# Kernel tuning notes

Hardware: AMD Instinct MI355X
Metric: run time of the kernel (lower is better)

## Reference

```python
import jax, jax.numpy as jnp
import numpy as np

B, S, D, H = 4, 1024, 1024, 16
DK = D // H


def setup_inputs() -> dict:
    key = jax.random.key(0)
    ks = jax.random.split(key, 13)
    s = 1.0 / np.sqrt(D)
    return {
        "query": jax.random.normal(ks[0], (B, S, D), jnp.float32),
        "key": jax.random.normal(ks[1], (B, S, D), jnp.float32),
        "value": jax.random.normal(ks[2], (B, S, D), jnp.float32),
        "mask": jax.random.randint(ks[3], (B, H, S, S), 0, 2).astype(bool),
        "Wq": jax.random.normal(ks[4], (D, D), jnp.float32) * s,
        "bq": jnp.zeros((D,), jnp.float32),
        "Wk": jax.random.normal(ks[5], (D, D), jnp.float32) * s,
        "bk": jnp.zeros((D,), jnp.float32),
        "Wv": jax.random.normal(ks[6], (D, D), jnp.float32) * s,
        "bv": jnp.zeros((D,), jnp.float32),
        "Wo": jax.random.normal(ks[7], (D, D), jnp.float32) * s,
        "bo": jnp.zeros((D,), jnp.float32),
    }


def reference(query, key, value, mask, Wq, bq, Wk, bk, Wv, bv, Wo, bo):
    b = query.shape[0]
    # QKV projections, split heads: [B,S,D] -> [B,H,S,DK]
    q = (query @ Wq + bq).reshape(b, -1, H, DK).transpose(0, 2, 1, 3)
    k = (key @ Wk + bk).reshape(b, -1, H, DK).transpose(0, 2, 1, 3)
    v = (value @ Wv + bv).reshape(b, -1, H, DK).transpose(0, 2, 1, 3)
    # scaled dot-product attention with explicit [B,H,Sq,Sk] scores
    scores = jnp.einsum("bhqd,bhkd->bhqk", q, k) / jnp.sqrt(jnp.float32(DK))
    scores = jnp.where(mask, -jnp.inf, scores)
    attn_weights = jax.nn.softmax(scores, axis=-1)
    attn_out = jnp.einsum("bhqk,bhkd->bhqd", attn_weights, v)
    # merge heads and project out; dropout is identity in eval mode
    attn_out = attn_out.transpose(0, 2, 1, 3).reshape(b, -1, D)
    out = attn_out @ Wo + bo
    return out, attn_weights
```

## Files before the change

### kernel.cpp

```cpp
#include <hip/hip_runtime.h>

typedef __attribute__((ext_vector_type(8))) __bf16   bf16x8;
typedef __attribute__((ext_vector_type(4))) __bf16   bf16x4;
typedef __attribute__((ext_vector_type(8))) _Float16 halfx8;
typedef __attribute__((ext_vector_type(4))) float    floatx4;
typedef __attribute__((ext_vector_type(4))) int      intx4;

#define S_  1024
#define D_  1024
#define H_  16
#define DK_ 64
#define B_  4
#define M_  4096

__device__ __forceinline__ void gload_lds16(const void* g, void* l) {
  __builtin_amdgcn_global_load_lds(
      (const __attribute__((address_space(1))) unsigned int*)g,
      (__attribute__((address_space(3))) unsigned int*)l, 16, 0, 0);
}

__global__ __launch_bounds__(256) void prep(
    const float* __restrict__ q, const float* __restrict__ k,
    const float* __restrict__ v, __bf16* __restrict__ X,
    const float* __restrict__ W0, const float* __restrict__ W1,
    const float* __restrict__ W2, const float* __restrict__ W3,
    __bf16* __restrict__ WT, const unsigned char* __restrict__ m,
    int* __restrict__ flag)
{
  __shared__ __align__(16) unsigned char shb[9216];
  const int bid = blockIdx.x;
  const int t = threadIdx.x;
  if (bid < 6144) {
    const int z = bid >> 11;
    const int bx = bid & 2047;
    const float* src = (z == 0) ? q : (z == 1) ? k : v;
    __bf16* dst = X + (size_t)z * 4194304;
    const size_t idx = ((size_t)bx * 256 + t) * 8;
    floatx4 a = *(const floatx4*)(src + idx);
    floatx4 b = *(const floatx4*)(src + idx + 4);
    bf16x8 o;
#pragma unroll
    for (int j = 0; j < 4; ++j) { o[j] = (__bf16)a[j]; o[4 + j] = (__bf16)b[j]; }
    *(bf16x8*)(dst + idx) = o;
  } else if (bid < 7168) {
    const int g = bid - 6144;
    const int z = g >> 8, yy = (g >> 4) & 15, xx = g & 15;
    const float* W = (z == 0) ? W0 : (z == 1) ? W1 : (z == 2) ? W2 : W3;
    __bf16* O = WT + (size_t)z * (D_ * (size_t)D_);
    __bf16* T = (__bf16*)shb;
    const int r0 = yy * 64, c0 = xx * 64;
#pragma unroll
    for (int it = 0; it < 4; ++it) {
      int idx = t * 4 + it * 1024;
      int r = idx >> 6, c = idx & 63;
      floatx4 a = *(const floatx4*)(W + (size_t)(r0 + r) * D_ + c0 + c);
      bf16x4 o;
#pragma unroll
      for (int j = 0; j < 4; ++j) o[j] = (__bf16)a[j];
      *(bf16x4*)(&T[r * 72 + c]) = o;
    }
    __syncthreads();
#pragma unroll
    for (int it = 0; it < 2; ++it) {
      int idx = t * 8 + it * 2048;
      int orow = idx >> 6, oc = idx & 63;
      bf16x8 vv;
#pragma unroll
      for (int j = 0; j < 8; ++j) vv[j] = T[(oc + j) * 72 + orow];
      *(bf16x8*)(O + (size_t)(c0 + orow) * D_ + (r0 + oc)) = vv;
    }
  } else {
    unsigned* sacc = (unsigned*)shb;
    unsigned acc = 0;
    for (int i = t; i < 4096; i += 256)
      if (i & 3) acc |= m[i];
    sacc[t] = acc;
    __syncthreads();
    if (t == 0) {
      unsigned tot = 0;
      for (int i = 0; i < 256; ++i) tot |= sacc[i];
      flag[0] = tot ? 1 : 0;
    }
  }
}

template <int MODE>
__device__ __forceinline__ void gemm_body(
    const __bf16* __restrict__ X, const __bf16* __restrict__ WT,
    const float* __restrict__ bias, void* __restrict__ outp, __bf16* sh,
    const int m0, const int n0)
{
  __bf16* As = sh;
  __bf16* Bs = sh + 128 * 64;
  const int t = threadIdx.x;
  const int w = t >> 6, lane = t & 63, quad = lane >> 4, cl = lane & 15;
  const int wm = w >> 1, wn = w & 1;
  const int srow = lane >> 3, scol = (lane & 7) * 8;

  floatx4 acc[4][4];
#pragma unroll
  for (int i = 0; i < 4; ++i)
#pragma unroll
    for (int j = 0; j < 4; ++j) acc[i][j] = (floatx4){0.f, 0.f, 0.f, 0.f};

  for (int kt = 0; kt < 16; ++kt) {
    const int k0 = kt * 64;
    __syncthreads();
#pragma unroll
    for (int it = 0; it < 4; ++it) {
      const int ch = it * 4 + w;
      gload_lds16(X  + (size_t)(m0 + ch * 8 + srow) * D_ + k0 + scol, As + ch * 512);
      gload_lds16(WT + (size_t)(n0 + ch * 8 + srow) * D_ + k0 + scol, Bs + ch * 512);
    }
    __syncthreads();
#pragma unroll
    for (int ks = 0; ks < 2; ++ks) {
      bf16x8 a[4], b[4];
#pragma unroll
      for (int mt = 0; mt < 4; ++mt)
        a[mt] = *(const bf16x8*)(&As[(wm * 64 + mt * 16 + cl) * 64 + ks * 32 + quad * 8]);
#pragma unroll
      for (int nt = 0; nt < 4; ++nt)
        b[nt] = *(const bf16x8*)(&Bs[(wn * 64 + nt * 16 + cl) * 64 + ks * 32 + quad * 8]);
#pragma unroll
      for (int mt = 0; mt < 4; ++mt)
#pragma unroll
        for (int nt = 0; nt < 4; ++nt)
          acc[mt][nt] = __builtin_amdgcn_mfma_f32_16x16x32_bf16(a[mt], b[nt], acc[mt][nt], 0, 0, 0);
    }
  }

  if (MODE <= 2) {
#pragma unroll
    for (int mt = 0; mt < 4; ++mt)
#pragma unroll
      for (int nt = 0; nt < 4; ++nt) {
        const int nl = n0 + wn * 64 + nt * 16 + cl;
        const float bv = bias[nl];
#pragma unroll
        for (int r = 0; r < 4; ++r) {
          const int ml = m0 + wm * 64 + mt * 16 + quad * 4 + r;
          float v = acc[mt][nt][r] + bv;
          if (MODE == 0) {
            ((float*)outp)[(size_t)ml * D_ + nl] = v;
          } else {
            if (MODE == 1) v *= 0.125f;
            const int bb = ml >> 10, ss = ml & 1023, hh = nl >> 6, dd = nl & 63;
            ((_Float16*)outp)[(size_t)((bb * H_ + hh) * S_ + ss) * DK_ + dd] = (_Float16)v;
          }
        }
      }
  } else {
    __syncthreads();
    __bf16* T = sh + w * (64 * 72);
    const int hbase = n0 + wn * 64;
#pragma unroll
    for (int mt = 0; mt < 4; ++mt)
#pragma unroll
      for (int nt = 0; nt < 4; ++nt) {
        const int nl = hbase + nt * 16 + cl;
        const float bv = bias[nl];
        const int dk = nt * 16 + cl;
#pragma unroll
        for (int r = 0; r < 4; ++r) {
          const int sl = mt * 16 + quad * 4 + r;
          T[dk * 72 + sl] = (__bf16)(acc[mt][nt][r] + bv);
        }
      }
    __syncthreads();
    const int bb = m0 >> 10;
    const int hh = hbase >> 6;
    __bf16* out = (__bf16*)outp;
#pragma unroll
    for (int i = 0; i < 8; ++i) {
      int idx = lane * 8 + i * 512;
      int dk = idx >> 6, sl = idx & 63;
      bf16x8 v = *(const bf16x8*)(&T[dk * 72 + sl]);
      int sg = (m0 & 1023) + wm * 64 + sl;
      *(bf16x8*)(out + (size_t)((bb * H_ + hh) * DK_ + dk) * S_ + sg) = v;
    }
  }
}

__global__ __launch_bounds__(256) void gemm_qkv(
    const __bf16* __restrict__ Xbf, const __bf16* __restrict__ wt,
    const float* __restrict__ bq, const float* __restrict__ bk,
    const float* __restrict__ bv,
    void* __restrict__ Qo, void* __restrict__ Ko, void* __restrict__ Vto)
{
  __shared__ __bf16 sh[18432];
  const int z = blockIdx.z;
  const int m0 = blockIdx.x * 128, n0 = blockIdx.y * 128;
  if (z == 0)      gemm_body<1>(Xbf,               wt,               bq, Qo,  sh, m0, n0);
  else if (z == 1) gemm_body<2>(Xbf + 4194304,     wt + 1048576,     bk, Ko,  sh, m0, n0);
  else             gemm_body<3>(Xbf + 2 * 4194304, wt + 2 * 1048576, bv, Vto, sh, m0, n0);
}

__global__ __launch_bounds__(256) void epilogue(
    const __bf16* __restrict__ AO, const __bf16* __restrict__ WT,
    const float* __restrict__ bo, float* __restrict__ outO,
    float* __restrict__ attnW, const __bf16* __restrict__ pp,
    const float* __restrict__ l)
{
  __shared__ __bf16 sh[18432];
  const int bid = blockIdx.x;
  if (bid < 256) {
    gemm_body<0>(AO, WT, bo, (void*)outO, sh, (bid & 31) * 128, (bid >> 5) * 128);
  } else {
    const int t = threadIdx.x;
    const int g = bid - 256;
    const int row = g * 2 + (t >> 7);
    const int c = (t & 127) * 8;
    const float lv = l[row];
    const float rl = (lv > 0.f) ? 1.0f / lv : 0.f;
    bf16x8 v = *(const bf16x8*)(pp + (size_t)row * S_ + c);
    floatx4 lo, hi;
#pragma unroll
    for (int j = 0; j < 4; ++j) { lo[j] = (float)v[j] * rl; hi[j] = (float)v[4 + j] * rl; }
    *(floatx4*)(attnW + (size_t)row * S_ + c) = lo;
    *(floatx4*)(attnW + (size_t)row * S_ + c + 4) = hi;
  }
}

__global__ __launch_bounds__(256, 4) void attn_kernel(
    const _Float16* __restrict__ Q, const _Float16* __restrict__ K,
    const __bf16* __restrict__ Vt, const unsigned char* __restrict__ maskB,
    const int* __restrict__ mflag, float* __restrict__ attnW,
    __bf16* __restrict__ pp, __bf16* __restrict__ AO,
    float* __restrict__ lout, const int sflag)
{
  __shared__ __align__(16) unsigned char smem[36864];
  _Float16*      Qs  = (_Float16*)smem;
  unsigned char* Ms  = smem;
  _Float16*      Ks  = (_Float16*)(smem + 9216);
  __bf16*        Vts = (__bf16*)(smem + 18432);
  __bf16*        Ps  = (__bf16*)(smem + 27648);

  const int t = threadIdx.x;
  const int w = t >> 6, lane = t & 63, quad = lane >> 4, cl = lane & 15;
  const int o = blockIdx.x + blockIdx.y * 16;
  const int f = (o & 7) * 128 + (o >> 3);
  const int q0 = (f & 15) * 64;
  const int bh = f >> 4;
  const bool mbyte = (*mflag != 0);
  const int* maskI = (const int*)maskB;
  const long maskbase = (long)bh * S_ * S_;

  {
    const _Float16* g = Q + (size_t)(bh * S_ + q0) * DK_;
#pragma unroll
    for (int it = 0; it < 2; ++it) {
      int idx = t * 8 + it * 2048;
      *(halfx8*)(&Qs[(idx >> 6) * 72 + (idx & 63)]) = *(const halfx8*)(g + idx);
    }
  }

  halfx8 kreg0, kreg1;
  bf16x8 vreg0, vreg1;
  intx4  mregs[4];
  const _Float16* Kbase  = K  + (size_t)bh * S_ * DK_;
  const __bf16*   Vbase  = Vt + (size_t)bh * DK_ * S_;

#define LOAD_TILE(KT)                                                              \
  {                                                                                \
    const int k0_ = (KT) * 64;                                                     \
    const _Float16* gk = Kbase + (size_t)k0_ * DK_;                                \
    kreg0 = *(const halfx8*)(gk + t * 8);                                          \
    kreg1 = *(const halfx8*)(gk + t * 8 + 2048);                                   \
    const __bf16* gv = Vbase + k0_;                                                \
    vreg0 = *(const bf16x8*)(gv + (size_t)(t >> 3) * S_ + (t & 7) * 8);            \
    vreg1 = *(const bf16x8*)(gv + (size_t)((t >> 3) + 32) * S_ + (t & 7) * 8);     \
    if (mbyte) {                                                                   \
      mregs[0] = *(const intx4*)(maskB + maskbase +                                \
                   (size_t)(q0 + (t >> 2)) * S_ + k0_ + (t & 3) * 16);             \
    } else {                                                                       \
      const int* mrowp = maskI + maskbase + (size_t)(q0 + (t >> 2)) * S_ + k0_ +   \
                         (t & 3) * 16;                                             \
      _Pragma("unroll")                                                            \
      for (int it_ = 0; it_ < 4; ++it_)                                            \
        mregs[it_] = *(const intx4*)(mrowp + it_ * 4);                             \
    }                                                                              \
  }

  LOAD_TILE(0);
  __syncthreads();
  const halfx8 a0 = *(const halfx8*)(&Qs[(w * 16 + cl) * 72 + quad * 8]);
  const halfx8 a1 = *(const halfx8*)(&Qs[(w * 16 + cl) * 72 + 32 + quad * 8]);

  float lacc[4] = {0.f, 0.f, 0.f, 0.f};
  floatx4 acc_o[4];
#pragma unroll
  for (int i = 0; i < 4; ++i) acc_o[i] = (floatx4){0.f, 0.f, 0.f, 0.f};
  __bf16* Psw = Ps + w * (16 * 72);

  for (int kt = 0; kt < 16; ++kt) {
    const int k0 = kt * 64;
    __syncthreads();

    *(halfx8*)(&Ks[(t >> 3) * 72 + (t & 7) * 8])        = kreg0;
    *(halfx8*)(&Ks[((t >> 3) + 32) * 72 + (t & 7) * 8]) = kreg1;
    *(bf16x8*)(&Vts[(t >> 3) * 72 + (t & 7) * 8])        = vreg0;
    *(bf16x8*)(&Vts[((t >> 3) + 32) * 72 + (t & 7) * 8]) = vreg1;
    {
      unsigned m16 = 0;
      if (mbyte) {
#pragma unroll
        for (int i = 0; i < 4; ++i) {
          unsigned v = (unsigned)mregs[0][i];
          m16 |= ((v & 0x000000ffu) ? 1u : 0u) << (i * 4 + 0);
          m16 |= ((v & 0x0000ff00u) ? 1u : 0u) << (i * 4 + 1);
          m16 |= ((v & 0x00ff0000u) ? 1u : 0u) << (i * 4 + 2);
          m16 |= ((v & 0xff000000u) ? 1u : 0u) << (i * 4 + 3);
        }
      } else {
#pragma unroll
        for (int it = 0; it < 4; ++it)
#pragma unroll
          for (int j = 0; j < 4; ++j)
            m16 |= (mregs[it][j] ? 1u : 0u) << (it * 4 + j);
      }
      ((unsigned short*)Ms)[(t >> 2) * 4 + (t & 3)] = (unsigned short)m16;
    }
    __syncthreads();

    unsigned long long mrow[4];
#pragma unroll
    for (int r = 0; r < 4; ++r)
      mrow[r] = ((const unsigned long long*)Ms)[w * 16 + quad * 4 + r];

    if (kt < 15) LOAD_TILE(kt + 1);

#pragma unroll
    for (int nt = 0; nt < 4; ++nt) {
      floatx4 s = (floatx4){0.f, 0.f, 0.f, 0.f};
      halfx8 b0 = *(const halfx8*)(&Ks[(nt * 16 + cl) * 72 + quad * 8]);
      halfx8 b1 = *(const halfx8*)(&Ks[(nt * 16 + cl) * 72 + 32 + quad * 8]);
      __builtin_amdgcn_s_setprio(1);
      s = __builtin_amdgcn_mfma_f32_16x16x32_f16(a0, b0, s, 0, 0, 0);
      s = __builtin_amdgcn_mfma_f32_16x16x32_f16(a1, b1, s, 0, 0, 0);
      __builtin_amdgcn_s_setprio(0);
#pragma unroll
      for (int r = 0; r < 4; ++r) {
        const int mk = (int)((mrow[r] >> (nt * 16 + cl)) & 1ull);
        float sv = s[r];
        sv = (sv < 25.f) ? sv : 25.f;
        float p = mk ? 0.0f : __expf(sv);
        __bf16 pb = (__bf16)p;
        lacc[r] += (float)pb;
        Psw[(quad * 4 + r) * 72 + nt * 16 + cl] = pb;
      }
    }

    __builtin_amdgcn_s_setprio(1);
#pragma unroll
    for (int ks = 0; ks < 2; ++ks) {
      bf16x8 a = *(const bf16x8*)(&Psw[cl * 72 + ks * 32 + quad * 8]);
#pragma unroll
      for (int nt2 = 0; nt2 < 4; ++nt2) {
        bf16x8 b = *(const bf16x8*)(&Vts[(nt2 * 16 + cl) * 72 + ks * 32 + quad * 8]);
        acc_o[nt2] = __builtin_amdgcn_mfma_f32_16x16x32_bf16(a, b, acc_o[nt2], 0, 0, 0);
      }
    }
    __builtin_amdgcn_s_setprio(0);

    if (sflag) {
      __bf16* g = pp + ((size_t)(bh * S_ + q0 + w * 16)) * S_ + k0;
#pragma unroll
      for (int i = 0; i < 2; ++i) {
        int idx = lane * 8 + i * 512;
        int r = idx >> 6, c = idx & 63;
        *(bf16x8*)(g + (size_t)r * S_ + c) = *(const bf16x8*)(&Psw[r * 72 + c]);
      }
    } else {
      float* g = attnW + ((long)(bh * S_ + q0 + w * 16)) * S_ + k0;
#pragma unroll
      for (int i = 0; i < 2; ++i) {
        int idx = lane * 8 + i * 512;
        int r = idx >> 6, c = idx & 63;
        bf16x8 v = *(const bf16x8*)(&Psw[r * 72 + c]);
        floatx4 lo, hi;
#pragma unroll
        for (int j = 0; j < 4; ++j) { lo[j] = (float)v[j]; hi[j] = (float)v[4 + j]; }
        *(floatx4*)(g + (long)r * S_ + c) = lo;
        *(floatx4*)(g + (long)r * S_ + c + 4) = hi;
      }
    }
  }
#undef LOAD_TILE

  const int bb = bh >> 4, hh = bh & 15;
#pragma unroll
  for (int r = 0; r < 4; ++r) {
    float v = lacc[r];
    v += __shfl_xor(v, 1); v += __shfl_xor(v, 2);
    v += __shfl_xor(v, 4); v += __shfl_xor(v, 8);
    const int rowg = q0 + w * 16 + quad * 4 + r;
    if (cl == 0) lout[bh * S_ + rowg] = v;
    const float rl = (v > 0.f) ? 1.0f / v : 0.f;
#pragma unroll
    for (int nt2 = 0; nt2 < 4; ++nt2) {
      float o2 = acc_o[nt2][r] * rl;
      AO[(size_t)(bb * S_ + rowg) * D_ + hh * DK_ + nt2 * 16 + cl] = (__bf16)o2;
    }
  }
}

__global__ __launch_bounds__(256) void norm_inplace(float* __restrict__ attnW,
                                                    const float* __restrict__ l)
{
  const int row = blockIdx.x;
  const float lv = l[row];
  const float rl = (lv > 0.f) ? 1.0f / lv : 0.f;
  const size_t base = (size_t)row * S_ + threadIdx.x * 4;
  floatx4 v = *(const floatx4*)(attnW + base);
#pragma unroll
  for (int j = 0; j < 4; ++j) v[j] *= rl;
  *(floatx4*)(attnW + base) = v;
}

__global__ __launch_bounds__(256) void gemm_out(
    const __bf16* __restrict__ X, const __bf16* __restrict__ WT,
    const float* __restrict__ bias, float* __restrict__ outp)
{
  __shared__ __bf16 sh[18432];
  gemm_body<0>(X, WT, bias, (void*)outp, sh, blockIdx.x * 128, blockIdx.y * 128);
}

extern "C" void kernel_launch(void* const* d_in, const int* in_sizes, int n_in,
                              void* d_out, int out_size, void* d_ws, size_t ws_size,
                              hipStream_t stream)
{
  (void)in_sizes; (void)n_in; (void)out_size;
  const float* query = (const float*)d_in[0];
  const float* key   = (const float*)d_in[1];
  const float* value = (const float*)d_in[2];
  const unsigned char* mask = (const unsigned char*)d_in[3];
  const float* Wq = (const float*)d_in[4];
  const float* bq = (const float*)d_in[5];
  const float* Wk = (const float*)d_in[6];
  const float* bk = (const float*)d_in[7];
  const float* Wv = (const float*)d_in[8];
  const float* bv = (const float*)d_in[9];
  const float* Wo = (const float*)d_in[10];
  const float* bo = (const float*)d_in[11];

  __bf16* ws = (__bf16*)d_ws;
  __bf16*   wt   = ws;
  _Float16* Qws  = (_Float16*)(ws + 4  * 1048576);
  _Float16* Kws  = (_Float16*)(ws + 8  * 1048576);
  __bf16*   Vtws = ws + 12 * 1048576;
  __bf16*   AOws = ws + 16 * 1048576;
  __bf16*   Xbf  = ws + 20 * 1048576;
  float*    lws  = (float*)(ws + 32 * 1048576);
  int*      mfl  = (int*)(ws + 32 * 1048576 + 131072);
  __bf16*   pp   = ws + 33 * 1048576;

  const int sflag = (ws_size >= 97ULL * 1048576ULL * 2ULL) ? 1 : 0;

  float* outO  = (float*)d_out;
  float* attnW = outO + 4 * 1048576;

  prep<<<7169, 256, 0, stream>>>(query, key, value, Xbf, Wq, Wk, Wv, Wo, wt, mask, mfl);
  gemm_qkv<<<dim3(32, 8, 3), 256, 0, stream>>>(Xbf, wt, bq, bk, bv,
                                               (void*)Qws, (void*)Kws, (void*)Vtws);
  attn_kernel<<<dim3(16, 64), 256, 0, stream>>>(Qws, Kws, Vtws, mask, mfl,
                                                attnW, pp, AOws, lws, sflag);
  if (sflag) {
    epilogue<<<33024, 256, 0, stream>>>(AOws, wt + 3 * 1048576, bo, outO, attnW, pp, lws);
  } else {
    norm_inplace<<<65536, 256, 0, stream>>>(attnW, lws);
    gemm_out<<<dim3(32, 8), 256, 0, stream>>>(AOws, wt + 3 * 1048576, bo, outO);
  }
}
```

Baseline: 679.1 us.

## Keep full unnormalized P row tile in LDS and write normalized attention weights directly

The attention kernel now keeps the whole 64x1024 bf16 probability tile in LDS (about 148KB) instead of a small per-step buffer. After the key loop it normalizes each row by its reciprocal sum and writes final fp32 attention weights once. This removes the bf16 scratch round trip (or the fp32 write plus in-place renormalization pass) and the separate epilogue/norm kernel. In exchange, the LDS footprint limits each CU to one block with four waves, which cuts occupancy and latency hiding in the attention loop, and the output-projection GEMM now runs as a separate launch.

```diff
diff --git a/kernel.cpp b/kernel.cpp
--- a/kernel.cpp
+++ b/kernel.cpp
@@ -196,45 +196,27 @@
   else             gemm_body<3>(Xbf + 2 * 4194304, wt + 2 * 1048576, bv, Vto, sh, m0, n0);
 }
 
-__global__ __launch_bounds__(256) void epilogue(
-    const __bf16* __restrict__ AO, const __bf16* __restrict__ WT,
-    const float* __restrict__ bo, float* __restrict__ outO,
-    float* __restrict__ attnW, const __bf16* __restrict__ pp,
-    const float* __restrict__ l)
+__global__ __launch_bounds__(256) void gemm_out(
+    const __bf16* __restrict__ X, const __bf16* __restrict__ WT,
+    const float* __restrict__ bias, float* __restrict__ outp)
 {
   __shared__ __bf16 sh[18432];
-  const int bid = blockIdx.x;
-  if (bid < 256) {
-    gemm_body<0>(AO, WT, bo, (void*)outO, sh, (bid & 31) * 128, (bid >> 5) * 128);
-  } else {
-    const int t = threadIdx.x;
-    const int g = bid - 256;
-    const int row = g * 2 + (t >> 7);
-    const int c = (t & 127) * 8;
-    const float lv = l[row];
-    const float rl = (lv > 0.f) ? 1.0f / lv : 0.f;
-    bf16x8 v = *(const bf16x8*)(pp + (size_t)row * S_ + c);
-    floatx4 lo, hi;
-#pragma unroll
-    for (int j = 0; j < 4; ++j) { lo[j] = (float)v[j] * rl; hi[j] = (float)v[4 + j] * rl; }
-    *(floatx4*)(attnW + (size_t)row * S_ + c) = lo;
-    *(floatx4*)(attnW + (size_t)row * S_ + c + 4) = hi;
-  }
-}
-
-__global__ __launch_bounds__(256, 4) void attn_kernel(
+  gemm_body<0>(X, WT, bias, (void*)outp, sh, blockIdx.x * 128, blockIdx.y * 128);
+}
+
+__global__ __launch_bounds__(256, 1) void attn_kernel(
     const _Float16* __restrict__ Q, const _Float16* __restrict__ K,
     const __bf16* __restrict__ Vt, const unsigned char* __restrict__ maskB,
     const int* __restrict__ mflag, float* __restrict__ attnW,
-    __bf16* __restrict__ pp, __bf16* __restrict__ AO,
-    float* __restrict__ lout, const int sflag)
-{
-  __shared__ __align__(16) unsigned char smem[36864];
+    __bf16* __restrict__ AO)
+{
+  __shared__ __align__(16) unsigned char smem[151296];
+  __bf16*        P   = (__bf16*)smem;
   _Float16*      Qs  = (_Float16*)smem;
-  unsigned char* Ms  = smem;
-  _Float16*      Ks  = (_Float16*)(smem + 9216);
-  __bf16*        Vts = (__bf16*)(smem + 18432);
-  __bf16*        Ps  = (__bf16*)(smem + 27648);
+  _Float16*      Ks  = (_Float16*)(smem + 132096);
+  __bf16*        Vts = (__bf16*)(smem + 141312);
+  unsigned char* Ms  = smem + 150528;
+  float*         rls = (float*)(smem + 151040);
 
   const int t = threadIdx.x;
   const int w = t >> 6, lane = t & 63, quad = lane >> 4, cl = lane & 15;
@@ -291,7 +273,7 @@
   floatx4 acc_o[4];
 #pragma unroll
   for (int i = 0; i < 4; ++i) acc_o[i] = (floatx4){0.f, 0.f, 0.f, 0.f};
-  __bf16* Psw = Ps + w * (16 * 72);
+  __bf16* Pw = P + (size_t)(w * 16) * 1032;
 
   for (int kt = 0; kt < 16; ++kt) {
     const int k0 = kt * 64;
@@ -347,14 +329,14 @@
         float p = mk ? 0.0f : __expf(sv);
         __bf16 pb = (__bf16)p;
         lacc[r] += (float)pb;
-        Psw[(quad * 4 + r) * 72 + nt * 16 + cl] = pb;
+        Pw[(quad * 4 + r) * 1032 + k0 + nt * 16 + cl] = pb;
       }
     }
 
     __builtin_amdgcn_s_setprio(1);
 #pragma unroll
     for (int ks = 0; ks < 2; ++ks) {
-      bf16x8 a = *(const bf16x8*)(&Psw[cl * 72 + ks * 32 + quad * 8]);
+      bf16x8 a = *(const bf16x8*)(&Pw[cl * 1032 + k0 + ks * 32 + quad * 8]);
 #pragma unroll
       for (int nt2 = 0; nt2 < 4; ++nt2) {
         bf16x8 b = *(const bf16x8*)(&Vts[(nt2 * 16 + cl) * 72 + ks * 32 + quad * 8]);
@@ -362,29 +344,6 @@
       }
     }
     __builtin_amdgcn_s_setprio(0);
-
-    if (sflag) {
-      __bf16* g = pp + ((size_t)(bh * S_ + q0 + w * 16)) * S_ + k0;
-#pragma unroll
-      for (int i = 0; i < 2; ++i) {
-        int idx = lane * 8 + i * 512;
-        int r = idx >> 6, c = idx & 63;
-        *(bf16x8*)(g + (size_t)r * S_ + c) = *(const bf16x8*)(&Psw[r * 72 + c]);
-      }
-    } else {
-      float* g = attnW + ((long)(bh * S_ + q0 + w * 16)) * S_ + k0;
-#pragma unroll
-      for (int i = 0; i < 2; ++i) {
-        int idx = lane * 8 + i * 512;
-        int r = idx >> 6, c = idx & 63;
-        bf16x8 v = *(const bf16x8*)(&Psw[r * 72 + c]);
-        floatx4 lo, hi;
-#pragma unroll
-        for (int j = 0; j < 4; ++j) { lo[j] = (float)v[j]; hi[j] = (float)v[4 + j]; }
-        *(floatx4*)(g + (long)r * S_ + c) = lo;
-        *(floatx4*)(g + (long)r * S_ + c + 4) = hi;
-      }
-    }
   }
 #undef LOAD_TILE
 
@@ -395,42 +354,36 @@
     v += __shfl_xor(v, 1); v += __shfl_xor(v, 2);
     v += __shfl_xor(v, 4); v += __shfl_xor(v, 8);
     const int rowg = q0 + w * 16 + quad * 4 + r;
-    if (cl == 0) lout[bh * S_ + rowg] = v;
     const float rl = (v > 0.f) ? 1.0f / v : 0.f;
+    if (cl == 0) rls[w * 16 + quad * 4 + r] = rl;
 #pragma unroll
     for (int nt2 = 0; nt2 < 4; ++nt2) {
       float o2 = acc_o[nt2][r] * rl;
       AO[(size_t)(bb * S_ + rowg) * D_ + hh * DK_ + nt2 * 16 + cl] = (__bf16)o2;
     }
   }
-}
-
-__global__ __launch_bounds__(256) void norm_inplace(float* __restrict__ attnW,
-                                                    const float* __restrict__ l)
-{
-  const int row = blockIdx.x;
-  const float lv = l[row];
-  const float rl = (lv > 0.f) ? 1.0f / lv : 0.f;
-  const size_t base = (size_t)row * S_ + threadIdx.x * 4;
-  floatx4 v = *(const floatx4*)(attnW + base);
-#pragma unroll
-  for (int j = 0; j < 4; ++j) v[j] *= rl;
-  *(floatx4*)(attnW + base) = v;
-}
-
-__global__ __launch_bounds__(256) void gemm_out(
-    const __bf16* __restrict__ X, const __bf16* __restrict__ WT,
-    const float* __restrict__ bias, float* __restrict__ outp)
-{
-  __shared__ __bf16 sh[18432];
-  gemm_body<0>(X, WT, bias, (void*)outp, sh, blockIdx.x * 128, blockIdx.y * 128);
+
+  for (int rr = 0; rr < 16; ++rr) {
+    const float rlv = rls[w * 16 + rr];
+    float* g = attnW + ((size_t)(bh * S_) + q0 + w * 16 + rr) * S_;
+    const __bf16* prow = &Pw[(size_t)rr * 1032];
+#pragma unroll
+    for (int i = 0; i < 4; ++i) {
+      const int c = lane * 4 + i * 256;
+      bf16x4 pv = *(const bf16x4*)(prow + c);
+      floatx4 ov;
+#pragma unroll
+      for (int j = 0; j < 4; ++j) ov[j] = (float)pv[j] * rlv;
+      *(floatx4*)(g + c) = ov;
+    }
+  }
 }
 
 extern "C" void kernel_launch(void* const* d_in, const int* in_sizes, int n_in,
                               void* d_out, int out_size, void* d_ws, size_t ws_size,
                               hipStream_t stream)
 {
-  (void)in_sizes; (void)n_in; (void)out_size;
+  (void)in_sizes; (void)n_in; (void)out_size; (void)ws_size;
   const float* query = (const float*)d_in[0];
   const float* key   = (const float*)d_in[1];
   const float* value = (const float*)d_in[2];
@@ -451,11 +404,7 @@
   __bf16*   Vtws = ws + 12 * 1048576;
   __bf16*   AOws = ws + 16 * 1048576;
   __bf16*   Xbf  = ws + 20 * 1048576;
-  float*    lws  = (float*)(ws + 32 * 1048576);
   int*      mfl  = (int*)(ws + 32 * 1048576 + 131072);
-  __bf16*   pp   = ws + 33 * 1048576;
-
-  const int sflag = (ws_size >= 97ULL * 1048576ULL * 2ULL) ? 1 : 0;
 
   float* outO  = (float*)d_out;
   float* attnW = outO + 4 * 1048576;
@@ -464,11 +413,6 @@
   gemm_qkv<<<dim3(32, 8, 3), 256, 0, stream>>>(Xbf, wt, bq, bk, bv,
                                                (void*)Qws, (void*)Kws, (void*)Vtws);
   attn_kernel<<<dim3(16, 64), 256, 0, stream>>>(Qws, Kws, Vtws, mask, mfl,
-                                                attnW, pp, AOws, lws, sflag);
-  if (sflag) {
-    epilogue<<<33024, 256, 0, stream>>>(AOws, wt + 3 * 1048576, bo, outO, attnW, pp, lws);
-  } else {
-    norm_inplace<<<65536, 256, 0, stream>>>(attnW, lws);
-    gemm_out<<<dim3(32, 8), 256, 0, stream>>>(AOws, wt + 3 * 1048576, bo, outO);
-  }
-}
+                                                attnW, AOws);
+  gemm_out<<<dim3(32, 8), 256, 0, stream>>>(AOws, wt + 3 * 1048576, bo, outO);
+}
```

Result: faster. 622.6 us (-8.3%).
